# Kernel tuning notes

Hardware: AMD Instinct MI355X
Metric: run time of the kernel (lower is better)

Reference implementation:

```python
import jax, jax.numpy as jnp
import numpy as np

N_NODES = 100000
N_EDGES = 1600000
N_IN = 256
N_H = 128


def setup_inputs() -> dict:
    key = jax.random.key(0)
    k1, k2, k3, k4 = jax.random.split(key, 4)
    x = jax.random.normal(k1, (N_NODES, N_IN), dtype=jnp.float32)
    edge_index = jax.random.randint(k2, (2, N_EDGES), 0, N_NODES, dtype=jnp.int64)
    # GCNConv weights (glorot-like scale) and biases
    W1 = jax.random.normal(k3, (N_IN, N_H), dtype=jnp.float32) / np.sqrt(N_IN)
    b1 = jnp.zeros((N_H,), dtype=jnp.float32)
    W2 = jax.random.normal(k4, (N_H, N_H), dtype=jnp.float32) / np.sqrt(N_H)
    b2 = jnp.zeros((N_H,), dtype=jnp.float32)
    return {"x": x, "W1": W1, "b1": b1, "W2": W2, "b2": b2, "edge_index": edge_index}


def _gcn_conv(x, W, b, row, col, n_nodes):
    """PyG GCNConv: add self-loops, symmetric norm D^-1/2 A D^-1/2, aggregate at target (col)."""
    h = x @ W  # [N, out]
    # degree including self-loop (edge_weight = 1): deg[i] = 1 + #incoming edges at target i
    deg = jnp.ones((n_nodes,), dtype=x.dtype).at[col].add(1.0)
    dinv = jax.lax.rsqrt(deg)
    # off-diagonal edges: msg j->i weighted by dinv[j]*dinv[i]
    norm = dinv[row] * dinv[col]  # [E]
    msg = h[row] * norm[:, None]  # [E, out]
    agg = jax.ops.segment_sum(msg, col, num_segments=n_nodes)
    # self-loop contribution: weight dinv[i]^2
    agg = agg + h * (dinv * dinv)[:, None]
    return agg + b


def reference(x, W1, b1, W2, b2, edge_index):
    row, col = edge_index[0], edge_index[1]
    n = x.shape[0]
    out = jax.nn.relu(_gcn_conv(x, W1, b1, row, col, n))
    out = _gcn_conv(out, W2, b2, row, col, n)
    return out
```

## Files before the change

### kernel.cpp

```cpp
#include <hip/hip_runtime.h>


#define NN 100000
#define NH 128
#define NB 196
#define SB 256

__device__ __forceinline__ float bf2f(unsigned int u) { return __uint_as_float(u << 16); }
__device__ __forceinline__ unsigned short f2bf(float f) {
    unsigned int u = __float_as_uint(f);
    u = (u + 0x7fffu + ((u >> 16) & 1u)) >> 16;
    return (unsigned short)u;
}

__device__ __forceinline__ void dma16(const void* g, void* l) {
    __builtin_amdgcn_global_load_lds(
        (const __attribute__((address_space(1))) unsigned int*)g,
        (__attribute__((address_space(3))) unsigned int*)l, 16, 0, 0);
}

__global__ __launch_bounds__(256) void k_hist(const int* __restrict__ col,
                                              int* __restrict__ blockCnt, int E, int chb) {
    __shared__ int h[NB];
    int t = threadIdx.x, blk = blockIdx.x;
    if (t < NB) h[t] = 0;
    __syncthreads();
    int s = blk * chb, en = min(E, s + chb);
    for (int e = s + t; e < en; e += 256) atomicAdd(&h[col[e] >> 9], 1);
    __syncthreads();
    if (t < NB) blockCnt[t * SB + blk] = h[t];
}

__global__ __launch_bounds__(256) void k_base(const int* __restrict__ blockCnt,
                                              int* __restrict__ base) {
    __shared__ int s[256];
    int t = threadIdx.x;
    int tot = 0;
    if (t < NB)
        for (int j = 0; j < SB; ++j) tot += blockCnt[t * SB + j];
    s[t] = tot;
    __syncthreads();
    for (int off = 1; off < 256; off <<= 1) {
        int v = (t >= off) ? s[t - off] : 0;
        __syncthreads();
        s[t] += v;
        __syncthreads();
    }
    if (t < NB) base[t] = s[t] - tot;
    if (t == NB - 1) base[NB] = s[t];
}

__global__ __launch_bounds__(256) void k_bscan(const int* __restrict__ blockCnt,
                                               const int* __restrict__ base,
                                               int* __restrict__ blockOff) {
    __shared__ int s[256];
    int t = threadIdx.x, b = blockIdx.x;
    int v = blockCnt[b * SB + t];
    s[t] = v;
    __syncthreads();
    for (int off = 1; off < 256; off <<= 1) {
        int u = (t >= off) ? s[t - off] : 0;
        __syncthreads();
        s[t] += u;
        __syncthreads();
    }
    blockOff[b * SB + t] = base[b] + s[t] - v;
}

__global__ __launch_bounds__(256) void k_scatter(const int* __restrict__ row,
                                                 const int* __restrict__ col,
                                                 const int* __restrict__ blockOff,
                                                 unsigned int* __restrict__ pairs,
                                                 int E, int chb) {
    __shared__ int cur[NB];
    __shared__ int bof[NB];
    int t = threadIdx.x, blk = blockIdx.x;
    if (t < NB) {
        cur[t] = 0;
        bof[t] = blockOff[t * SB + blk];
    }
    __syncthreads();
    int s = blk * chb, en = min(E, s + chb);
    for (int e = s + t; e < en; e += 256) {
        int c = col[e];
        int b = c >> 9;
        int r = atomicAdd(&cur[b], 1);
        pairs[bof[b] + r] = (unsigned int)row[e] | ((unsigned int)(c & 511) << 17);
    }
}

__global__ __launch_bounds__(512) void k_bin(const unsigned int* __restrict__ pairs,
                                             const int* __restrict__ base,
                                             unsigned int* __restrict__ csr,
                                             int* __restrict__ offs,
                                             float* __restrict__ dinv, int n) {
    __shared__ int cnt[512];
    __shared__ int s[512];
    int t = threadIdx.x, b = blockIdx.x;
    cnt[t] = 0;
    __syncthreads();
    int e0 = base[b], e1 = base[b + 1];
    for (int i = e0 + t; i < e1; i += 512) atomicAdd(&cnt[pairs[i] >> 17], 1);
    __syncthreads();
    int v = cnt[t];
    int node = b * 512 + t;
    if (node < n) dinv[node] = rsqrtf(1.0f + (float)v);
    s[t] = v;
    __syncthreads();
    for (int off = 1; off < 512; off <<= 1) {
        int u = (t >= off) ? s[t - off] : 0;
        __syncthreads();
        s[t] += u;
        __syncthreads();
    }
    int excl = s[t] - v;
    if (node <= n) offs[node] = e0 + excl;
    __syncthreads();
    cnt[t] = e0 + excl;
    __syncthreads();
    for (int i = e0 + t; i < e1; i += 512) {
        unsigned int p = pairs[i];
        int d = atomicAdd(&cnt[p >> 17], 1);
        csr[d] = p & 0x1FFFFu;
    }
}

__global__ void k_wprep(const float* __restrict__ W, unsigned short* __restrict__ Thi,
                        unsigned short* __restrict__ Tlo, int K) {
    int idx = blockIdx.x * 256 + threadIdx.x;
    if (idx >= K * 128) return;
    int k = idx >> 7, c = idx & 127;
    float w = W[idx];
    unsigned int u = __float_as_uint(w) & 0xffff0000u;
    float rem = w - __uint_as_float(u);
    Thi[(size_t)c * K + k] = (unsigned short)(u >> 16);
    Tlo[(size_t)c * K + k] = (unsigned short)(__float_as_uint(rem) >> 16);
}

template <int K>
__global__ __launch_bounds__(256) void k_gemm_mfma(const float* __restrict__ A,
                                                   const unsigned short* __restrict__ Bhi,
                                                   const unsigned short* __restrict__ Blo,
                                                   const float* __restrict__ dinv,
                                                   unsigned short* __restrict__ C, int M) {
    using bf16x8 = __attribute__((ext_vector_type(8))) short;
    using f32x4  = __attribute__((ext_vector_type(4))) float;
    constexpr int T = K / 32;
    __shared__ uint4 sA4[2][1024];
    __shared__ uint4 sB4[2][2][512];

    const int lane = threadIdx.x & 63;
    const int wv   = threadIdx.x >> 6;
    const int r    = lane & 15;
    const int kb   = lane >> 4;
    const int rowBase = blockIdx.x * 128;

    f32x4 acc[2][8];
#pragma unroll
    for (int m = 0; m < 2; ++m)
#pragma unroll
        for (int t = 0; t < 8; ++t) acc[m][t] = (f32x4){0.f, 0.f, 0.f, 0.f};

#pragma unroll
    for (int ks = 0; ks < T; ++ks) {
        const int buf = ks & 1;
        const int kk  = ks * 32;
#pragma unroll
        for (int c = 0; c < 4; ++c) {
            int sb = wv * 256 + c * 64;
            int s  = sb + lane;
            int akb = s >> 8, aj = (s >> 7) & 1, ar = s & 127;
            int gr = rowBase + ar; if (gr >= M) gr = M - 1;
            dma16(A + (size_t)gr * K + kk + akb * 8 + aj * 4, &sA4[buf][sb]);
        }
#pragma unroll
        for (int hl = 0; hl < 2; ++hl) {
            const unsigned short* Bp = hl ? Blo : Bhi;
#pragma unroll
            for (int c = 0; c < 2; ++c) {
                int sb = wv * 128 + c * 64;
                int s  = sb + lane;
                int bkb = s >> 7, bcol = s & 127;
                dma16(Bp + (size_t)bcol * K + kk + bkb * 8, &sB4[buf][hl][sb]);
            }
        }
        __syncthreads();
        bf16x8 ah[2], al[2];
#pragma unroll
        for (int m = 0; m < 2; ++m) {
            int rowl = wv * 32 + m * 16 + r;
            uint4 u0 = sA4[buf][kb * 256 + rowl];
            uint4 u1 = sA4[buf][kb * 256 + 128 + rowl];
            float f[8];
            *(uint4*)&f[0] = u0;
            *(uint4*)&f[4] = u1;
#pragma unroll
            for (int j = 0; j < 8; ++j) {
                float x = f[j];
                unsigned int u = __float_as_uint(x) & 0xffff0000u;
                ah[m][j] = (short)(u >> 16);
                al[m][j] = (short)(__float_as_uint(x - __uint_as_float(u)) >> 16);
            }
        }
#pragma unroll
        for (int t = 0; t < 8; ++t) {
            int col = t * 16 + r;
            bf16x8 bh = *(const bf16x8*)&sB4[buf][0][kb * 128 + col];
            bf16x8 bl = *(const bf16x8*)&sB4[buf][1][kb * 128 + col];
#pragma unroll
            for (int m = 0; m < 2; ++m) {
                acc[m][t] = __builtin_amdgcn_mfma_f32_16x16x32_bf16(ah[m], bh, acc[m][t], 0, 0, 0);
                acc[m][t] = __builtin_amdgcn_mfma_f32_16x16x32_bf16(al[m], bh, acc[m][t], 0, 0, 0);
                acc[m][t] = __builtin_amdgcn_mfma_f32_16x16x32_bf16(ah[m], bl, acc[m][t], 0, 0, 0);
            }
        }
    }
    const int wrow = rowBase + wv * 32;
#pragma unroll
    for (int m = 0; m < 2; ++m) {
#pragma unroll
        for (int q = 0; q < 4; ++q) {
            int orow = wrow + m * 16 + kb * 4 + q;
            if (orow < M) {
                float dv = dinv[orow];
#pragma unroll
                for (int t = 0; t < 8; ++t)
                    C[(size_t)orow * 128 + t * 16 + r] = f2bf(acc[m][t][q] * dv);
            }
        }
    }
}

template <bool RELU>
__global__ __launch_bounds__(256) void k_agg(const unsigned short* __restrict__ hb,
                                             const float* __restrict__ dinv,
                                             const int* __restrict__ off,
                                             const unsigned int* __restrict__ csr,
                                             const float* __restrict__ bias,
                                             float* __restrict__ out, int n) {
    int node = blockIdx.x * 8 + (threadIdx.x >> 5);
    int lane = threadIdx.x & 31;
    if (node >= n) return;
    float di = dinv[node];
    uint2 us = *(const uint2*)(hb + ((size_t)node << 7) + lane * 4);
    float a0 = bf2f(us.x & 0xffffu);
    float a1 = bf2f(us.x >> 16);
    float a2 = bf2f(us.y & 0xffffu);
    float a3 = bf2f(us.y >> 16);
    int e  = off[node];
    int e1 = off[node + 1];
    for (; e + 4 <= e1; e += 4) {
        unsigned int s0 = csr[e + 0];
        unsigned int s1 = csr[e + 1];
        unsigned int s2 = csr[e + 2];
        unsigned int s3 = csr[e + 3];
        uint2 u0 = *(const uint2*)(hb + ((size_t)s0 << 7) + lane * 4);
        uint2 u1 = *(const uint2*)(hb + ((size_t)s1 << 7) + lane * 4);
        uint2 u2 = *(const uint2*)(hb + ((size_t)s2 << 7) + lane * 4);
        uint2 u3 = *(const uint2*)(hb + ((size_t)s3 << 7) + lane * 4);
        a0 += bf2f(u0.x & 0xffffu); a1 += bf2f(u0.x >> 16);
        a2 += bf2f(u0.y & 0xffffu); a3 += bf2f(u0.y >> 16);
        a0 += bf2f(u1.x & 0xffffu); a1 += bf2f(u1.x >> 16);
        a2 += bf2f(u1.y & 0xffffu); a3 += bf2f(u1.y >> 16);
        a0 += bf2f(u2.x & 0xffffu); a1 += bf2f(u2.x >> 16);
        a2 += bf2f(u2.y & 0xffffu); a3 += bf2f(u2.y >> 16);
        a0 += bf2f(u3.x & 0xffffu); a1 += bf2f(u3.x >> 16);
        a2 += bf2f(u3.y & 0xffffu); a3 += bf2f(u3.y >> 16);
    }
    for (; e < e1; ++e) {
        unsigned int s = csr[e];
        uint2 u = *(const uint2*)(hb + ((size_t)s << 7) + lane * 4);
        a0 += bf2f(u.x & 0xffffu); a1 += bf2f(u.x >> 16);
        a2 += bf2f(u.y & 0xffffu); a3 += bf2f(u.y >> 16);
    }
    float4 b = *(const float4*)&bias[lane * 4];
    a0 = a0 * di + b.x;
    a1 = a1 * di + b.y;
    a2 = a2 * di + b.z;
    a3 = a3 * di + b.w;
    if (RELU) {
        a0 = fmaxf(a0, 0.f); a1 = fmaxf(a1, 0.f);
        a2 = fmaxf(a2, 0.f); a3 = fmaxf(a3, 0.f);
    }
    *(float4*)(out + ((size_t)node << 7) + lane * 4) = make_float4(a0, a1, a2, a3);
}

extern "C" void kernel_launch(void* const* d_in, const int* in_sizes, int n_in,
                              void* d_out, int out_size, void* d_ws, size_t ws_size,
                              hipStream_t stream) {
    const float* x  = (const float*)d_in[0];
    const float* W1 = (const float*)d_in[1];
    const float* b1 = (const float*)d_in[2];
    const float* W2 = (const float*)d_in[3];
    const float* b2 = (const float*)d_in[4];
    const int*   ei = (const int*)d_in[5];

    const int n = NN;
    const int E = in_sizes[5] / 2;
    const int* row = ei;
    const int* col = ei + E;

    char* ws = (char*)d_ws;
    size_t o = 0;
    auto alloc = [&](size_t bytes) {
        void* p = ws + o;
        o = (o + bytes + 255) & ~(size_t)255;
        return p;
    };
    int*            blockCnt = (int*)alloc((size_t)NB * SB * 4);
    int*            blockOff = (int*)alloc((size_t)NB * SB * 4);
    int*            base     = (int*)alloc((size_t)(NB + 1) * 4);
    int*            offs     = (int*)alloc((size_t)(n + 1) * 4);
    float*          dinv     = (float*)alloc((size_t)n * 4);
    unsigned int*   pairs    = (unsigned int*)alloc((size_t)E * 4);
    unsigned int*   csr      = (unsigned int*)alloc((size_t)E * 4);
    unsigned short* bufH     = (unsigned short*)alloc((size_t)n * NH * 2);
    float*          bufG     = (float*)alloc((size_t)n * NH * 4);
    unsigned short* wt1hi    = (unsigned short*)alloc(256 * 128 * 2);
    unsigned short* wt1lo    = (unsigned short*)alloc(256 * 128 * 2);
    unsigned short* wt2hi    = (unsigned short*)alloc(128 * 128 * 2);
    unsigned short* wt2lo    = (unsigned short*)alloc(128 * 128 * 2);

    const int chb = (E + SB - 1) / SB;

    k_wprep<<<(256 * 128 + 255) / 256, 256, 0, stream>>>(W1, wt1hi, wt1lo, 256);
    k_wprep<<<(128 * 128 + 255) / 256, 256, 0, stream>>>(W2, wt2hi, wt2lo, 128);

    k_hist<<<SB, 256, 0, stream>>>(col, blockCnt, E, chb);
    k_base<<<1, 256, 0, stream>>>(blockCnt, base);
    k_bscan<<<NB, 256, 0, stream>>>(blockCnt, base, blockOff);
    k_scatter<<<SB, 256, 0, stream>>>(row, col, blockOff, pairs, E, chb);
    k_bin<<<NB, 512, 0, stream>>>(pairs, base, csr, offs, dinv, n);

    int aggBlocks = (n + 7) / 8;
    int gemmBlocks = (n + 127) / 128;
    k_gemm_mfma<256><<<gemmBlocks, 256, 0, stream>>>(x, wt1hi, wt1lo, dinv, bufH, n);
    k_agg<true><<<aggBlocks, 256, 0, stream>>>(bufH, dinv, offs, csr, b1, bufG, n);
    k_gemm_mfma<128><<<gemmBlocks, 256, 0, stream>>>(bufG, wt2hi, wt2lo, dinv, bufH, n);
    k_agg<false><<<aggBlocks, 256, 0, stream>>>(bufH, dinv, offs, csr, b2, (float*)d_out, n);
}
```

Before: 270.1 us.

## Store layer-1 activations in bf16 and widen aggregation to 16 lanes per node

The layer-1 aggregation now writes its ReLU output as bf16 instead of fp32. A new bf16-input MFMA GEMM streams that buffer directly into LDS, which halves the intermediate traffic and removes the fp32 A-operand handling in the second GEMM. The aggregation kernel also switches from 32 lanes loading 8 bytes to 16 lanes loading 16 bytes per node, which gives wider gathers and more nodes per block. The cost is extra rounding of the hidden activations to bf16, which could reduce accuracy.

```diff
diff --git a/kernel.cpp b/kernel.cpp
--- a/kernel.cpp
+++ b/kernel.cpp
@@ -231,22 +231,101 @@
     }
 }
 
-template <bool RELU>
+template <int K>
+__global__ __launch_bounds__(256) void k_gemm_bf16(const unsigned short* __restrict__ A,
+                                                   const unsigned short* __restrict__ Bhi,
+                                                   const unsigned short* __restrict__ Blo,
+                                                   const float* __restrict__ dinv,
+                                                   unsigned short* __restrict__ C, int M) {
+    using bf16x8 = __attribute__((ext_vector_type(8))) short;
+    using f32x4  = __attribute__((ext_vector_type(4))) float;
+    constexpr int T = K / 32;
+    __shared__ uint4 sA2[2][512];
+    __shared__ uint4 sB4[2][2][512];
+
+    const int lane = threadIdx.x & 63;
+    const int wv   = threadIdx.x >> 6;
+    const int r    = lane & 15;
+    const int kb   = lane >> 4;
+    const int rowBase = blockIdx.x * 128;
+
+    f32x4 acc[2][8];
+#pragma unroll
+    for (int m = 0; m < 2; ++m)
+#pragma unroll
+        for (int t = 0; t < 8; ++t) acc[m][t] = (f32x4){0.f, 0.f, 0.f, 0.f};
+
+#pragma unroll
+    for (int ks = 0; ks < T; ++ks) {
+        const int buf = ks & 1;
+        const int kk  = ks * 32;
+#pragma unroll
+        for (int c = 0; c < 2; ++c) {
+            int sb = wv * 128 + c * 64;
+            int s  = sb + lane;
+            int akb = s >> 7, ar = s & 127;
+            int gr = rowBase + ar; if (gr >= M) gr = M - 1;
+            dma16(A + (size_t)gr * K + kk + akb * 8, &sA2[buf][sb]);
+        }
+#pragma unroll
+        for (int hl = 0; hl < 2; ++hl) {
+            const unsigned short* Bp = hl ? Blo : Bhi;
+#pragma unroll
+            for (int c = 0; c < 2; ++c) {
+                int sb = wv * 128 + c * 64;
+                int s  = sb + lane;
+                int bkb = s >> 7, bcol = s & 127;
+                dma16(Bp + (size_t)bcol * K + kk + bkb * 8, &sB4[buf][hl][sb]);
+            }
+        }
+        __syncthreads();
+#pragma unroll
+        for (int t = 0; t < 8; ++t) {
+            int col = t * 16 + r;
+            bf16x8 bh = *(const bf16x8*)&sB4[buf][0][kb * 128 + col];
+            bf16x8 bl = *(const bf16x8*)&sB4[buf][1][kb * 128 + col];
+#pragma unroll
+            for (int m = 0; m < 2; ++m) {
+                bf16x8 a = *(const bf16x8*)&sA2[buf][kb * 128 + wv * 32 + m * 16 + r];
+                acc[m][t] = __builtin_amdgcn_mfma_f32_16x16x32_bf16(a, bh, acc[m][t], 0, 0, 0);
+                acc[m][t] = __builtin_amdgcn_mfma_f32_16x16x32_bf16(a, bl, acc[m][t], 0, 0, 0);
+            }
+        }
+    }
+    const int wrow = rowBase + wv * 32;
+#pragma unroll
+    for (int m = 0; m < 2; ++m) {
+#pragma unroll
+        for (int q = 0; q < 4; ++q) {
+            int orow = wrow + m * 16 + kb * 4 + q;
+            if (orow < M) {
+                float dv = dinv[orow];
+#pragma unroll
+                for (int t = 0; t < 8; ++t)
+                    C[(size_t)orow * 128 + t * 16 + r] = f2bf(acc[m][t][q] * dv);
+            }
+        }
+    }
+}
+
+template <bool RELU, bool BF16OUT>
 __global__ __launch_bounds__(256) void k_agg(const unsigned short* __restrict__ hb,
                                              const float* __restrict__ dinv,
                                              const int* __restrict__ off,
                                              const unsigned int* __restrict__ csr,
                                              const float* __restrict__ bias,
-                                             float* __restrict__ out, int n) {
-    int node = blockIdx.x * 8 + (threadIdx.x >> 5);
-    int lane = threadIdx.x & 31;
+                                             void* __restrict__ outv, int n) {
+    int gid  = blockIdx.x * 256 + threadIdx.x;
+    int node = gid >> 4;
+    int lane = gid & 15;
     if (node >= n) return;
     float di = dinv[node];
-    uint2 us = *(const uint2*)(hb + ((size_t)node << 7) + lane * 4);
-    float a0 = bf2f(us.x & 0xffffu);
-    float a1 = bf2f(us.x >> 16);
-    float a2 = bf2f(us.y & 0xffffu);
-    float a3 = bf2f(us.y >> 16);
+    uint4 us = *(const uint4*)(hb + ((size_t)node << 7) + lane * 8);
+    float a[8];
+    a[0] = bf2f(us.x & 0xffffu); a[1] = bf2f(us.x >> 16);
+    a[2] = bf2f(us.y & 0xffffu); a[3] = bf2f(us.y >> 16);
+    a[4] = bf2f(us.z & 0xffffu); a[5] = bf2f(us.z >> 16);
+    a[6] = bf2f(us.w & 0xffffu); a[7] = bf2f(us.w >> 16);
     int e  = off[node];
     int e1 = off[node + 1];
     for (; e + 4 <= e1; e += 4) {
@@ -254,35 +333,57 @@
         unsigned int s1 = csr[e + 1];
         unsigned int s2 = csr[e + 2];
         unsigned int s3 = csr[e + 3];
-        uint2 u0 = *(const uint2*)(hb + ((size_t)s0 << 7) + lane * 4);
-        uint2 u1 = *(const uint2*)(hb + ((size_t)s1 << 7) + lane * 4);
-        uint2 u2 = *(const uint2*)(hb + ((size_t)s2 << 7) + lane * 4);
-        uint2 u3 = *(const uint2*)(hb + ((size_t)s3 << 7) + lane * 4);
-        a0 += bf2f(u0.x & 0xffffu); a1 += bf2f(u0.x >> 16);
-        a2 += bf2f(u0.y & 0xffffu); a3 += bf2f(u0.y >> 16);
-        a0 += bf2f(u1.x & 0xffffu); a1 += bf2f(u1.x >> 16);
-        a2 += bf2f(u1.y & 0xffffu); a3 += bf2f(u1.y >> 16);
-        a0 += bf2f(u2.x & 0xffffu); a1 += bf2f(u2.x >> 16);
-        a2 += bf2f(u2.y & 0xffffu); a3 += bf2f(u2.y >> 16);
-        a0 += bf2f(u3.x & 0xffffu); a1 += bf2f(u3.x >> 16);
-        a2 += bf2f(u3.y & 0xffffu); a3 += bf2f(u3.y >> 16);
+        uint4 u0 = *(const uint4*)(hb + ((size_t)s0 << 7) + lane * 8);
+        uint4 u1 = *(const uint4*)(hb + ((size_t)s1 << 7) + lane * 8);
+        uint4 u2 = *(const uint4*)(hb + ((size_t)s2 << 7) + lane * 8);
+        uint4 u3 = *(const uint4*)(hb + ((size_t)s3 << 7) + lane * 8);
+        a[0] += bf2f(u0.x & 0xffffu); a[1] += bf2f(u0.x >> 16);
+        a[2] += bf2f(u0.y & 0xffffu); a[3] += bf2f(u0.y >> 16);
+        a[4] += bf2f(u0.z & 0xffffu); a[5] += bf2f(u0.z >> 16);
+        a[6] += bf2f(u0.w & 0xffffu); a[7] += bf2f(u0.w >> 16);
+        a[0] += bf2f(u1.x & 0xffffu); a[1] += bf2f(u1.x >> 16);
+        a[2] += bf2f(u1.y & 0xffffu); a[3] += bf2f(u1.y >> 16);
+        a[4] += bf2f(u1.z & 0xffffu); a[5] += bf2f(u1.z >> 16);
+        a[6] += bf2f(u1.w & 0xffffu); a[7] += bf2f(u1.w >> 16);
+        a[0] += bf2f(u2.x & 0xffffu); a[1] += bf2f(u2.x >> 16);
+        a[2] += bf2f(u2.y & 0xffffu); a[3] += bf2f(u2.y >> 16);
+        a[4] += bf2f(u2.z & 0xffffu); a[5] += bf2f(u2.z >> 16);
+        a[6] += bf2f(u2.w & 0xffffu); a[7] += bf2f(u2.w >> 16);
+        a[0] += bf2f(u3.x & 0xffffu); a[1] += bf2f(u3.x >> 16);
+        a[2] += bf2f(u3.y & 0xffffu); a[3] += bf2f(u3.y >> 16);
+        a[4] += bf2f(u3.z & 0xffffu); a[5] += bf2f(u3.z >> 16);
+        a[6] += bf2f(u3.w & 0xffffu); a[7] += bf2f(u3.w >> 16);
     }
     for (; e < e1; ++e) {
         unsigned int s = csr[e];
-        uint2 u = *(const uint2*)(hb + ((size_t)s << 7) + lane * 4);
-        a0 += bf2f(u.x & 0xffffu); a1 += bf2f(u.x >> 16);
-        a2 += bf2f(u.y & 0xffffu); a3 += bf2f(u.y >> 16);
-    }
-    float4 b = *(const float4*)&bias[lane * 4];
-    a0 = a0 * di + b.x;
-    a1 = a1 * di + b.y;
-    a2 = a2 * di + b.z;
-    a3 = a3 * di + b.w;
+        uint4 u = *(const uint4*)(hb + ((size_t)s << 7) + lane * 8);
+        a[0] += bf2f(u.x & 0xffffu); a[1] += bf2f(u.x >> 16);
+        a[2] += bf2f(u.y & 0xffffu); a[3] += bf2f(u.y >> 16);
+        a[4] += bf2f(u.z & 0xffffu); a[5] += bf2f(u.z >> 16);
+        a[6] += bf2f(u.w & 0xffffu); a[7] += bf2f(u.w >> 16);
+    }
+    float4 b0 = *(const float4*)&bias[lane * 8];
+    float4 b1 = *(const float4*)&bias[lane * 8 + 4];
+    a[0] = a[0] * di + b0.x; a[1] = a[1] * di + b0.y;
+    a[2] = a[2] * di + b0.z; a[3] = a[3] * di + b0.w;
+    a[4] = a[4] * di + b1.x; a[5] = a[5] * di + b1.y;
+    a[6] = a[6] * di + b1.z; a[7] = a[7] * di + b1.w;
     if (RELU) {
-        a0 = fmaxf(a0, 0.f); a1 = fmaxf(a1, 0.f);
-        a2 = fmaxf(a2, 0.f); a3 = fmaxf(a3, 0.f);
-    }
-    *(float4*)(out + ((size_t)node << 7) + lane * 4) = make_float4(a0, a1, a2, a3);
+#pragma unroll
+        for (int j = 0; j < 8; ++j) a[j] = fmaxf(a[j], 0.f);
+    }
+    if (BF16OUT) {
+        uint4 o;
+        o.x = (unsigned int)f2bf(a[0]) | ((unsigned int)f2bf(a[1]) << 16);
+        o.y = (unsigned int)f2bf(a[2]) | ((unsigned int)f2bf(a[3]) << 16);
+        o.z = (unsigned int)f2bf(a[4]) | ((unsigned int)f2bf(a[5]) << 16);
+        o.w = (unsigned int)f2bf(a[6]) | ((unsigned int)f2bf(a[7]) << 16);
+        *(uint4*)((unsigned short*)outv + ((size_t)node << 7) + lane * 8) = o;
+    } else {
+        float* op = (float*)outv + ((size_t)node << 7) + lane * 8;
+        *(float4*)op       = make_float4(a[0], a[1], a[2], a[3]);
+        *(float4*)(op + 4) = make_float4(a[4], a[5], a[6], a[7]);
+    }
 }
 
 extern "C" void kernel_launch(void* const* d_in, const int* in_sizes, int n_in,
@@ -315,7 +416,7 @@
     unsigned int*   pairs    = (unsigned int*)alloc((size_t)E * 4);
     unsigned int*   csr      = (unsigned int*)alloc((size_t)E * 4);
     unsigned short* bufH     = (unsigned short*)alloc((size_t)n * NH * 2);
-    float*          bufG     = (float*)alloc((size_t)n * NH * 4);
+    unsigned short* bufG     = (unsigned short*)alloc((size_t)n * NH * 2);
     unsigned short* wt1hi    = (unsigned short*)alloc(256 * 128 * 2);
     unsigned short* wt1lo    = (unsigned short*)alloc(256 * 128 * 2);
     unsigned short* wt2hi    = (unsigned short*)alloc(128 * 128 * 2);
@@ -332,10 +433,10 @@
     k_scatter<<<SB, 256, 0, stream>>>(row, col, blockOff, pairs, E, chb);
     k_bin<<<NB, 512, 0, stream>>>(pairs, base, csr, offs, dinv, n);
 
-    int aggBlocks = (n + 7) / 8;
+    int aggBlocks = (n + 15) / 16;
     int gemmBlocks = (n + 127) / 128;
     k_gemm_mfma<256><<<gemmBlocks, 256, 0, stream>>>(x, wt1hi, wt1lo, dinv, bufH, n);
-    k_agg<true><<<aggBlocks, 256, 0, stream>>>(bufH, dinv, offs, csr, b1, bufG, n);
-    k_gemm_mfma<128><<<gemmBlocks, 256, 0, stream>>>(bufG, wt2hi, wt2lo, dinv, bufH, n);
-    k_agg<false><<<aggBlocks, 256, 0, stream>>>(bufH, dinv, offs, csr, b2, (float*)d_out, n);
-}
+    k_agg<true, true><<<aggBlocks, 256, 0, stream>>>(bufH, dinv, offs, csr, b1, bufG, n);
+    k_gemm_bf16<128><<<gemmBlocks, 256, 0, stream>>>(bufG, wt2hi, wt2lo, dinv, bufH, n);
+    k_agg<false, false><<<aggBlocks, 256, 0, stream>>>(bufH, dinv, offs, csr, b2, d_out, n);
+}
```

Measured after the change: 254.8 us. -5.6%, faster.
